# Performance work log

Hardware: AMD Instinct MI355X
Metric: run time of the kernel (lower is better)

Reference implementation:

```python
import jax, jax.numpy as jnp
import numpy as np

NP = 14      # patches per side
PS = 16      # patch size
L = 12       # transformer blocks
H = 12       # heads
DH = 64      # head dim
D = 768      # hidden dim
S = NP * NP + 1  # 197 tokens
EPS = 1e-5   # torch LayerNorm default eps


def _pos_embed():
    # pos[i, j] = sin(i / 10000^(2*(j//2)/D)) for even j, cos(...) for odd j
    i = jnp.arange(S, dtype=jnp.float32)[:, None]
    j = jnp.arange(D)
    angle = i / jnp.power(jnp.float32(10000.0), (2.0 * (j // 2).astype(jnp.float32)) / D)
    return jnp.where(j % 2 == 0, jnp.sin(angle), jnp.cos(angle))  # [S, D]


def _ln(x, g, b):
    m = jnp.mean(x, axis=-1, keepdims=True)
    v = jnp.mean((x - m) ** 2, axis=-1, keepdims=True)
    return (x - m) / jnp.sqrt(v + EPS) * g + b


def setup_inputs() -> dict:
    key = jax.random.key(0)
    ks = iter(jax.random.split(key, 16))
    r = lambda shape, s=0.02: jax.random.normal(next(ks), shape, dtype=jnp.float32) * s
    return {
        'image': jax.random.normal(next(ks), (32, 3, 224, 224), dtype=jnp.float32),
        'W_embed': r((D, 3 * PS * PS)),
        'b_embed': jnp.zeros((D,), jnp.float32),
        'cls': r((1, D), 1.0),
        'Wq': r((L, H, DH, DH)), 'bq': jnp.zeros((L, H, DH), jnp.float32),
        'Wk': r((L, H, DH, DH)), 'bk': jnp.zeros((L, H, DH), jnp.float32),
        'Wv': r((L, H, DH, DH)), 'bv': jnp.zeros((L, H, DH), jnp.float32),
        'ln1_g': jnp.ones((L, D), jnp.float32), 'ln1_b': jnp.zeros((L, D), jnp.float32),
        'ln2_g': jnp.ones((L, D), jnp.float32), 'ln2_b': jnp.zeros((L, D), jnp.float32),
        'W1': r((L, 4 * D, D)), 'b1': jnp.zeros((L, 4 * D), jnp.float32),
        'W2': r((L, D, 4 * D)), 'b2': jnp.zeros((L, D), jnp.float32),
        'Wh': r((1000, D)), 'bh': jnp.zeros((1000,), jnp.float32),
    }


def reference(image, W_embed, b_embed, cls, Wq, bq, Wk, bk, Wv, bv,
              ln1_g, ln1_b, ln2_g, ln2_b, W1, b1, W2, b2, Wh, bh):
    B = image.shape[0]
    # patchify: (B,C,H,W) -> (B, NP*NP, C*PS*PS), token order row-major over (i,j), flatten order (C,ps,ps)
    patches = image.reshape(B, 3, NP, PS, NP, PS).transpose(0, 2, 4, 1, 3, 5).reshape(B, NP * NP, 3 * PS * PS)
    tokens = patches @ W_embed.T + b_embed                      # [B, 196, D]
    tokens = jnp.concatenate([jnp.broadcast_to(cls[None], (B, 1, D)), tokens], axis=1)  # [B, S, D]
    x = tokens + _pos_embed()[None]
    scale = 1.0 / jnp.sqrt(jnp.float32(DH))
    for l in range(L):
        h = _ln(x, ln1_g[l], ln1_b[l]).reshape(B, S, H, DH)
        q = jnp.einsum('bshd,hed->bshe', h, Wq[l]) + bq[l]
        k = jnp.einsum('bshd,hed->bshe', h, Wk[l]) + bk[l]
        v = jnp.einsum('bshd,hed->bshe', h, Wv[l]) + bv[l]
        att = jax.nn.softmax(jnp.einsum('bshe,bthe->bhst', q, k) * scale, axis=-1)
        o = jnp.einsum('bhst,bthe->bshe', att, v).reshape(B, S, D)
        x = x + o
        h2 = _ln(x, ln2_g[l], ln2_b[l])
        m = jax.nn.gelu(h2 @ W1[l].T + b1[l], approximate=False)  # torch nn.GELU = exact erf
        x = x + m @ W2[l].T + b2[l]
    return x[:, 0] @ Wh.T + bh  # [B, 1000]
```

## Files before the change

### kernel.cpp

```cpp
#include <hip/hip_runtime.h>
#include <math.h>

#define BB 32
#define SS 197
#define DD 768
#define HH 12
#define DHD 64
#define LL 12
#define FF 3072
#define NPATCH 196
#define NTOK (BB * SS)
#define MPAD 6400
#define LNEPS 1e-5f

typedef short bf8_t __attribute__((ext_vector_type(8)));
typedef float f4_t  __attribute__((ext_vector_type(4)));
typedef unsigned short u16x8 __attribute__((ext_vector_type(8)));

__device__ __forceinline__ unsigned short f2bf(float x) {
    unsigned u = __float_as_uint(x);
    return (unsigned short)((u + 0x8000u) >> 16);
}
__device__ __forceinline__ float bf_lo(unsigned u) { return __uint_as_float(u << 16); }

__device__ __forceinline__ void gl_lds16(const void* g, void* l) {
    __builtin_amdgcn_global_load_lds((const __attribute__((address_space(1))) unsigned int*)g,
                                     (__attribute__((address_space(3))) unsigned int*)l, 16, 0, 0);
}

__global__ __launch_bounds__(256) void k_conv(const float* __restrict__ a,
                                              unsigned short* __restrict__ o, int n4) {
    for (int i = blockIdx.x * 256 + threadIdx.x; i < n4; i += gridDim.x * 256) {
        float4 v = ((const float4*)a)[i];
        ushort4 r;
        r.x = f2bf(v.x); r.y = f2bf(v.y); r.z = f2bf(v.z); r.w = f2bf(v.w);
        ((ushort4*)o)[i] = r;
    }
}

__global__ __launch_bounds__(256) void k_conv2(const float* __restrict__ a1,
                                               unsigned short* __restrict__ o1, int n1,
                                               const float* __restrict__ a2,
                                               unsigned short* __restrict__ o2, int n2) {
    for (int i = blockIdx.x * 256 + threadIdx.x; i < n1 + n2; i += gridDim.x * 256) {
        const float* a = (i < n1) ? a1 : a2;
        unsigned short* o = (i < n1) ? o1 : o2;
        int j = (i < n1) ? i : i - n1;
        float4 v = ((const float4*)a)[j];
        ushort4 r;
        r.x = f2bf(v.x); r.y = f2bf(v.y); r.z = f2bf(v.z); r.w = f2bf(v.w);
        ((ushort4*)o)[j] = r;
    }
}

__global__ __launch_bounds__(256) void k_patchify(const float* __restrict__ img,
                                                  unsigned short* __restrict__ P) {
    const int total = BB * NPATCH * DD;
    for (int idx = blockIdx.x * 256 + threadIdx.x; idx < total; idx += gridDim.x * 256) {
        int e = idx % DD;
        int rest = idx / DD;
        int p = rest % NPATCH;
        int b = rest / NPATCH;
        int c = e >> 8;
        int pi = (e >> 4) & 15;
        int pj = e & 15;
        int i = p / 14, j = p % 14;
        P[idx] = f2bf(img[(((size_t)b * 3 + c) * 224 + (i * 16 + pi)) * 224 + (j * 16 + pj)]);
    }
}

template <int EPI>
__global__ __launch_bounds__(256) void k_gemm_bf(const unsigned short* __restrict__ A,
                                                 const unsigned short* __restrict__ Bw,
                                                 const float* __restrict__ bias,
                                                 void* __restrict__ Cout,
                                                 int M, int N, int K) {
    __shared__ unsigned short As[128 * 32];
    __shared__ unsigned short Bs[128 * 32];
    const int tid = threadIdx.x;
    const int wave = tid >> 6, lane = tid & 63;
    const int m0 = blockIdx.y << 7, n0 = blockIdx.x << 7;

    const int r0 = tid >> 2, kp = (tid & 3) * 8;
    const unsigned short* gA0 = A + (size_t)(m0 + r0) * K + kp;
    const unsigned short* gA1 = A + (size_t)(m0 + 64 + r0) * K + kp;
    const unsigned short* gB0 = Bw + (size_t)(n0 + r0) * K + kp;
    const unsigned short* gB1 = Bw + (size_t)(n0 + 64 + r0) * K + kp;
    unsigned short* lA0 = &As[tid * 8];
    unsigned short* lA1 = &As[(tid + 256) * 8];
    unsigned short* lB0 = &Bs[tid * 8];
    unsigned short* lB1 = &Bs[(tid + 256) * 8];

    const int mh = (wave >> 1) << 6, nh = (wave & 1) << 6;
    const int lm = lane & 15, kq = lane >> 4;

    f4_t acc[4][4];
#pragma unroll
    for (int i = 0; i < 4; ++i)
#pragma unroll
        for (int j = 0; j < 4; ++j) acc[i][j] = (f4_t){0.f, 0.f, 0.f, 0.f};

    for (int k0 = 0; k0 < K; k0 += 32) {
        gl_lds16(gA0, lA0);
        gl_lds16(gA1, lA1);
        gl_lds16(gB0, lB0);
        gl_lds16(gB1, lB1);
        gA0 += 32; gA1 += 32; gB0 += 32; gB1 += 32;
        __syncthreads();
        bf8_t af[4], bfr[4];
#pragma unroll
        for (int mt = 0; mt < 4; ++mt)
            af[mt] = *(const bf8_t*)&As[(mh + mt * 16 + lm) * 32 + kq * 8];
#pragma unroll
        for (int nt = 0; nt < 4; ++nt)
            bfr[nt] = *(const bf8_t*)&Bs[(nh + nt * 16 + lm) * 32 + kq * 8];
#pragma unroll
        for (int mt = 0; mt < 4; ++mt)
#pragma unroll
            for (int nt = 0; nt < 4; ++nt)
                acc[mt][nt] = __builtin_amdgcn_mfma_f32_16x16x32_bf16(af[mt], bfr[nt],
                                                                      acc[mt][nt], 0, 0, 0);
        __syncthreads();
    }

    const int rbase = m0 + mh + kq * 4;
    const int cbase = n0 + nh + lm;
#pragma unroll
    for (int mt = 0; mt < 4; ++mt) {
#pragma unroll
        for (int nt = 0; nt < 4; ++nt) {
            const int col = cbase + nt * 16;
            const float bv = bias[col];
#pragma unroll
            for (int r = 0; r < 4; ++r) {
                const int row = rbase + mt * 16 + r;
                float val = acc[mt][nt][r] + bv;
                if (EPI == 0) {
                    size_t om = (size_t)(row / 196) * 197 + (row % 196) + 1;
                    ((float*)Cout)[om * DD + col] = val;
                } else if (EPI == 1) {
                    val = 0.5f * val * (1.f + erff(val * 0.7071067811865476f));
                    ((unsigned short*)Cout)[(size_t)row * N + col] = f2bf(val);
                } else {
                    if (row < M) ((float*)Cout)[(size_t)row * DD + col] += val;
                }
            }
        }
    }
}

__global__ __launch_bounds__(256) void k_gemm_sk(const unsigned short* __restrict__ A,
                                                 const unsigned short* __restrict__ Bw,
                                                 const float* __restrict__ bias,
                                                 float* __restrict__ Cout,
                                                 int M, int N, int K) {
    __shared__ unsigned short As[128 * 32];
    __shared__ unsigned short Bs[128 * 32];
    const int tid = threadIdx.x;
    const int wave = tid >> 6, lane = tid & 63;
    const int m0 = blockIdx.y << 7, n0 = blockIdx.x << 7;
    const int ksplit = K / gridDim.z;
    const int kbeg = blockIdx.z * ksplit;

    const int r0 = tid >> 2, kp = (tid & 3) * 8;
    const unsigned short* gA0 = A + (size_t)(m0 + r0) * K + kbeg + kp;
    const unsigned short* gA1 = A + (size_t)(m0 + 64 + r0) * K + kbeg + kp;
    const unsigned short* gB0 = Bw + (size_t)(n0 + r0) * K + kbeg + kp;
    const unsigned short* gB1 = Bw + (size_t)(n0 + 64 + r0) * K + kbeg + kp;
    unsigned short* lA0 = &As[tid * 8];
    unsigned short* lA1 = &As[(tid + 256) * 8];
    unsigned short* lB0 = &Bs[tid * 8];
    unsigned short* lB1 = &Bs[(tid + 256) * 8];

    const int mh = (wave >> 1) << 6, nh = (wave & 1) << 6;
    const int lm = lane & 15, kq = lane >> 4;

    f4_t acc[4][4];
#pragma unroll
    for (int i = 0; i < 4; ++i)
#pragma unroll
        for (int j = 0; j < 4; ++j) acc[i][j] = (f4_t){0.f, 0.f, 0.f, 0.f};

    for (int k0 = 0; k0 < ksplit; k0 += 32) {
        gl_lds16(gA0, lA0);
        gl_lds16(gA1, lA1);
        gl_lds16(gB0, lB0);
        gl_lds16(gB1, lB1);
        gA0 += 32; gA1 += 32; gB0 += 32; gB1 += 32;
        __syncthreads();
        bf8_t af[4], bfr[4];
#pragma unroll
        for (int mt = 0; mt < 4; ++mt)
            af[mt] = *(const bf8_t*)&As[(mh + mt * 16 + lm) * 32 + kq * 8];
#pragma unroll
        for (int nt = 0; nt < 4; ++nt)
            bfr[nt] = *(const bf8_t*)&Bs[(nh + nt * 16 + lm) * 32 + kq * 8];
#pragma unroll
        for (int mt = 0; mt < 4; ++mt)
#pragma unroll
            for (int nt = 0; nt < 4; ++nt)
                acc[mt][nt] = __builtin_amdgcn_mfma_f32_16x16x32_bf16(af[mt], bfr[nt],
                                                                      acc[mt][nt], 0, 0, 0);
        __syncthreads();
    }

    const int rbase = m0 + mh + kq * 4;
    const int cbase = n0 + nh + lm;
    const bool addb = (blockIdx.z == 0);
#pragma unroll
    for (int mt = 0; mt < 4; ++mt) {
#pragma unroll
        for (int nt = 0; nt < 4; ++nt) {
            const int col = cbase + nt * 16;
            const float bv = addb ? bias[col] : 0.f;
#pragma unroll
            for (int r = 0; r < 4; ++r) {
                const int row = rbase + mt * 16 + r;
                if (row < M)
                    unsafeAtomicAdd(&Cout[(size_t)row * DD + col], acc[mt][nt][r] + bv);
            }
        }
    }
}

__global__ __launch_bounds__(256) void k_qkv_mfma(const unsigned short* __restrict__ h,
                                                  const unsigned short* __restrict__ Wqb,
                                                  const unsigned short* __restrict__ Wkb,
                                                  const unsigned short* __restrict__ Wvb,
                                                  const float* __restrict__ bq,
                                                  const float* __restrict__ bk,
                                                  const float* __restrict__ bv,
                                                  unsigned short* __restrict__ qo,
                                                  unsigned short* __restrict__ ko,
                                                  unsigned short* __restrict__ vo) {
    __shared__ unsigned short As[2 * 128 * 32];
    __shared__ unsigned short Bs[3 * 2 * 64 * 32];
    const int head = blockIdx.x;
    const int m0 = blockIdx.y << 7;
    const int tid = threadIdx.x;
    const int wave = tid >> 6, lane = tid & 63;
    const int lm = lane & 15, kq = lane >> 4;

#pragma unroll
    for (int j = 0; j < 4; ++j) {
        int khalf = j >> 1;
        int rem = (j & 1) * 256 + tid;
        int row = rem >> 2, koff = (rem & 3) * 8;
        gl_lds16(h + (size_t)(m0 + row) * DD + head * 64 + khalf * 32 + koff,
                 &As[(j * 256 + tid) * 8]);
    }
    const unsigned short* Wq_h = Wqb + head * 4096;
    const unsigned short* Wk_h = Wkb + head * 4096;
    const unsigned short* Wv_h = Wvb + head * 4096;
#pragma unroll
    for (int j = 0; j < 6; ++j) {
        const unsigned short* src = (j < 2) ? Wq_h : ((j < 4) ? Wk_h : Wv_h);
        int cm = (j & 1) * 256 + tid;
        int khalf = cm >> 8;
        int rem2 = cm & 255;
        int row = rem2 >> 2, koff = (rem2 & 3) * 8;
        gl_lds16(src + row * 64 + khalf * 32 + koff, &Bs[(j * 256 + tid) * 8]);
    }
    __syncthreads();

    f4_t acc[2][12];
#pragma unroll
    for (int i = 0; i < 2; ++i)
#pragma unroll
        for (int j = 0; j < 12; ++j) acc[i][j] = (f4_t){0.f, 0.f, 0.f, 0.f};

#pragma unroll
    for (int kh = 0; kh < 2; ++kh) {
        bf8_t af[2], bfr[12];
#pragma unroll
        for (int mt = 0; mt < 2; ++mt)
            af[mt] = *(const bf8_t*)&As[kh * 4096 + (wave * 32 + mt * 16 + lm) * 32 + kq * 8];
#pragma unroll
        for (int nt = 0; nt < 12; ++nt)
            bfr[nt] = *(const bf8_t*)&Bs[(nt >> 2) * 4096 + kh * 2048 +
                                         ((nt & 3) * 16 + lm) * 32 + kq * 8];
#pragma unroll
        for (int mt = 0; mt < 2; ++mt)
#pragma unroll
            for (int nt = 0; nt < 12; ++nt)
                acc[mt][nt] = __builtin_amdgcn_mfma_f32_16x16x32_bf16(af[mt], bfr[nt],
                                                                      acc[mt][nt], 0, 0, 0);
    }

    const int rbase = m0 + wave * 32 + kq * 4;
#pragma unroll
    for (int mt = 0; mt < 2; ++mt) {
#pragma unroll
        for (int nt = 0; nt < 12; ++nt) {
            const int col = nt * 16 + lm;
            const int e = col & 63;
            const float* bsrc = (nt < 4) ? bq : ((nt < 8) ? bk : bv);
            unsigned short* dst = (nt < 4) ? qo : ((nt < 8) ? ko : vo);
            const float bval = bsrc[head * 64 + e];
#pragma unroll
            for (int r = 0; r < 4; ++r) {
                const int row = rbase + mt * 16 + r;
                if (row < NTOK)
                    dst[(size_t)row * DD + head * 64 + e] = f2bf(acc[mt][nt][r] + bval);
            }
        }
    }
}

__global__ __launch_bounds__(256) void k_posadd(float* __restrict__ x,
                                                const float* __restrict__ cls) {
    const int total = BB * SS * DD;
    const float LN1E4 = 9.210340371976184f;
    for (int idx = blockIdx.x * 256 + threadIdx.x; idx < total; idx += gridDim.x * 256) {
        int d = idx % DD;
        int s = (idx / DD) % SS;
        float ang = (float)s * __expf(-LN1E4 * (float)(2 * (d >> 1)) / 768.f);
        float pv = (d & 1) ? __cosf(ang) : __sinf(ang);
        if (s == 0) x[idx] = cls[d] + pv;
        else        x[idx] += pv;
    }
}

__global__ __launch_bounds__(256) void k_ln2(const float* __restrict__ x,
                                             const float* __restrict__ g,
                                             const float* __restrict__ bp,
                                             unsigned short* __restrict__ out) {
    const int row = blockIdx.x * 4 + (threadIdx.x >> 6);
    const int lane = threadIdx.x & 63;
    if (row >= NTOK) return;
    const float* xr = x + (size_t)row * DD + lane * 12;
    float4 a = ((const float4*)xr)[0];
    float4 b = ((const float4*)xr)[1];
    float4 c = ((const float4*)xr)[2];
    float s = a.x + a.y + a.z + a.w + b.x + b.y + b.z + b.w + c.x + c.y + c.z + c.w;
#pragma unroll
    for (int o = 32; o; o >>= 1) s += __shfl_xor(s, o);
    const float mean = s * (1.f / DD);
    float vr = 0.f, e0;
    e0 = a.x - mean; vr += e0 * e0; e0 = a.y - mean; vr += e0 * e0;
    e0 = a.z - mean; vr += e0 * e0; e0 = a.w - mean; vr += e0 * e0;
    e0 = b.x - mean; vr += e0 * e0; e0 = b.y - mean; vr += e0 * e0;
    e0 = b.z - mean; vr += e0 * e0; e0 = b.w - mean; vr += e0 * e0;
    e0 = c.x - mean; vr += e0 * e0; e0 = c.y - mean; vr += e0 * e0;
    e0 = c.z - mean; vr += e0 * e0; e0 = c.w - mean; vr += e0 * e0;
#pragma unroll
    for (int o = 32; o; o >>= 1) vr += __shfl_xor(vr, o);
    const float rstd = rsqrtf(vr * (1.f / DD) + LNEPS);

    const float4* g4 = (const float4*)(g + lane * 12);
    const float4* b4p = (const float4*)(bp + lane * 12);
    unsigned short* op = out + (size_t)row * DD + lane * 12;
    float4 gv, bv;
    ushort4 r;
    gv = g4[0]; bv = b4p[0];
    r.x = f2bf((a.x - mean) * rstd * gv.x + bv.x);
    r.y = f2bf((a.y - mean) * rstd * gv.y + bv.y);
    r.z = f2bf((a.z - mean) * rstd * gv.z + bv.z);
    r.w = f2bf((a.w - mean) * rstd * gv.w + bv.w);
    ((ushort4*)op)[0] = r;
    gv = g4[1]; bv = b4p[1];
    r.x = f2bf((b.x - mean) * rstd * gv.x + bv.x);
    r.y = f2bf((b.y - mean) * rstd * gv.y + bv.y);
    r.z = f2bf((b.z - mean) * rstd * gv.z + bv.z);
    r.w = f2bf((b.w - mean) * rstd * gv.w + bv.w);
    ((ushort4*)op)[1] = r;
    gv = g4[2]; bv = b4p[2];
    r.x = f2bf((c.x - mean) * rstd * gv.x + bv.x);
    r.y = f2bf((c.y - mean) * rstd * gv.y + bv.y);
    r.z = f2bf((c.z - mean) * rstd * gv.z + bv.z);
    r.w = f2bf((c.w - mean) * rstd * gv.w + bv.w);
    ((ushort4*)op)[2] = r;
}

__global__ __launch_bounds__(256) void k_attn3(const unsigned short* __restrict__ qg,
                                               const unsigned short* __restrict__ kg,
                                               const unsigned short* __restrict__ vg,
                                               float* __restrict__ x) {
    const int qt = blockIdx.x, head = blockIdx.y, b = blockIdx.z;
    const int tid = threadIdx.x, wv = tid >> 6, lane = tid & 63;
    const int lm = lane & 15, kq = lane >> 4;

    __shared__ __align__(16) unsigned short lds[29696];
    unsigned short* Kl = lds;
    unsigned short* Pl = lds;
    unsigned short* Vt = lds + 14848;

    const size_t tokbase = (size_t)b * SS;
    const unsigned short* kb = kg + tokbase * DD + head * 64;
    const unsigned short* vb = vg + tokbase * DD + head * 64;
    const unsigned short* qb = qg + tokbase * DD + head * 64;

#pragma unroll
    for (int it = 0; it < 7; ++it) {
        int c = it * 256 + tid;
        int kh = c / 896, rem = c - kh * 896;
        int t = rem >> 2, cc = rem & 3;
        gl_lds16(kb + (size_t)t * DD + kh * 32 + cc * 8, (char*)lds + c * 16);
    }
#pragma unroll
    for (int it = 0; it < 7; ++it) {
        int idx = it * 256 + tid;
        int t = idx >> 3, eg = idx & 7;
        if (t < SS) {
            u16x8 v8 = *(const u16x8*)(vb + (size_t)t * DD + eg * 8);
#pragma unroll
            for (int j = 0; j < 8; ++j) Vt[(eg * 8 + j) * 232 + t] = v8[j];
        } else {
#pragma unroll
            for (int j = 0; j < 8; ++j) Vt[(eg * 8 + j) * 232 + t] = 0;
        }
    }

    const int qrow = qt * 64 + wv * 16 + lm;
    bf8_t qf0 = *(const bf8_t*)(qb + (size_t)qrow * DD + kq * 8);
    bf8_t qf1 = *(const bf8_t*)(qb + (size_t)qrow * DD + 32 + kq * 8);

    __syncthreads();

    f4_t sacc[13];
#pragma unroll
    for (int tt = 0; tt < 13; ++tt) sacc[tt] = (f4_t){0.f, 0.f, 0.f, 0.f};
#pragma unroll
    for (int tt = 0; tt < 13; ++tt) {
        bf8_t a0 = *(const bf8_t*)&Kl[(tt * 16 + lm) * 32 + kq * 8];
        bf8_t a1 = *(const bf8_t*)&Kl[7168 + (tt * 16 + lm) * 32 + kq * 8];
        sacc[tt] = __builtin_amdgcn_mfma_f32_16x16x32_bf16(a0, qf0, sacc[tt], 0, 0, 0);
        sacc[tt] = __builtin_amdgcn_mfma_f32_16x16x32_bf16(a1, qf1, sacc[tt], 0, 0, 0);
    }

    float mx = -1e30f;
#pragma unroll
    for (int tt = 0; tt < 13; ++tt)
#pragma unroll
        for (int r = 0; r < 4; ++r) {
            float s = sacc[tt][r] * 0.125f;
            if (tt == 12 && (kq * 4 + r) >= 5) s = -1e30f;
            sacc[tt][r] = s;
            mx = fmaxf(mx, s);
        }
    mx = fmaxf(mx, __shfl_xor(mx, 16));
    mx = fmaxf(mx, __shfl_xor(mx, 32));
    float sum = 0.f;
#pragma unroll
    for (int tt = 0; tt < 13; ++tt)
#pragma unroll
        for (int r = 0; r < 4; ++r) {
            float p = __expf(sacc[tt][r] - mx);
            sacc[tt][r] = p;
            sum += p;
        }
    sum += __shfl_xor(sum, 16);
    sum += __shfl_xor(sum, 32);
    const float inv = 1.f / sum;

    __syncthreads();

    unsigned short* Pw = Pl + wv * 3712;
#pragma unroll
    for (int tt = 0; tt < 13; ++tt)
#pragma unroll
        for (int r = 0; r < 4; ++r)
            Pw[lm * 232 + tt * 16 + kq * 4 + r] = f2bf(sacc[tt][r]);
    *(short4*)&Pw[lm * 232 + 208 + kq * 4] = make_short4(0, 0, 0, 0);

    f4_t oacc[4];
#pragma unroll
    for (int et = 0; et < 4; ++et) oacc[et] = (f4_t){0.f, 0.f, 0.f, 0.f};
#pragma unroll
    for (int kc = 0; kc < 7; ++kc) {
        bf8_t pa = *(const bf8_t*)&Pw[lm * 232 + kc * 32 + kq * 8];
#pragma unroll
        for (int et = 0; et < 4; ++et) {
            bf8_t vv = *(const bf8_t*)&Vt[(et * 16 + lm) * 232 + kc * 32 + kq * 8];
            oacc[et] = __builtin_amdgcn_mfma_f32_16x16x32_bf16(pa, vv, oacc[et], 0, 0, 0);
        }
    }

    float invq[4];
#pragma unroll
    for (int r = 0; r < 4; ++r) invq[r] = __shfl(inv, kq * 4 + r);

    float* xp = x + tokbase * DD + head * 64;
#pragma unroll
    for (int r = 0; r < 4; ++r) {
        const int qgr = qt * 64 + wv * 16 + kq * 4 + r;
        if (qgr < SS) {
#pragma unroll
            for (int et = 0; et < 4; ++et)
                xp[(size_t)qgr * DD + et * 16 + lm] += oacc[et][r] * invq[r];
        }
    }
}

__global__ __launch_bounds__(256) void k_head(const float* __restrict__ x,
                                              const float* __restrict__ Wh,
                                              const float* __restrict__ bh,
                                              float* __restrict__ out) {
    const int b = blockIdx.y;
    const int c = blockIdx.x * 256 + threadIdx.x;
    __shared__ __align__(16) float xs[DD];
    const float* xr = x + (size_t)b * SS * DD;
    for (int d = threadIdx.x; d < DD; d += 256) xs[d] = xr[d];
    __syncthreads();
    if (c < 1000) {
        const float4* w4 = (const float4*)(Wh + (size_t)c * DD);
        float acc = 0.f;
#pragma unroll 4
        for (int d4 = 0; d4 < DD / 4; ++d4) {
            float4 w = w4[d4];
            const float4 xv = *(const float4*)&xs[d4 << 2];
            acc += xv.x * w.x + xv.y * w.y + xv.z * w.z + xv.w * w.w;
        }
        out[(size_t)b * 1000 + c] = acc + bh[c];
    }
}

extern "C" void kernel_launch(void* const* d_in, const int* in_sizes, int n_in,
                              void* d_out, int out_size, void* d_ws, size_t ws_size,
                              hipStream_t stream) {
    const float* image   = (const float*)d_in[0];
    const float* W_embed = (const float*)d_in[1];
    const float* b_embed = (const float*)d_in[2];
    const float* cls     = (const float*)d_in[3];
    const float* Wq      = (const float*)d_in[4];
    const float* bq      = (const float*)d_in[5];
    const float* Wk      = (const float*)d_in[6];
    const float* bk      = (const float*)d_in[7];
    const float* Wv      = (const float*)d_in[8];
    const float* bv      = (const float*)d_in[9];
    const float* ln1g    = (const float*)d_in[10];
    const float* ln1b    = (const float*)d_in[11];
    const float* ln2g    = (const float*)d_in[12];
    const float* ln2b    = (const float*)d_in[13];
    const float* W1      = (const float*)d_in[14];
    const float* b1      = (const float*)d_in[15];
    const float* W2      = (const float*)d_in[16];
    const float* b2      = (const float*)d_in[17];
    const float* Wh      = (const float*)d_in[18];
    const float* bh      = (const float*)d_in[19];
    float* out = (float*)d_out;

    float* x = (float*)d_ws;
    unsigned short* h_bf   = (unsigned short*)(x + (size_t)NTOK * DD);
    unsigned short* q_bf   = h_bf + (size_t)MPAD * DD;
    unsigned short* k_bf   = q_bf + (size_t)MPAD * DD;
    unsigned short* v_bf   = k_bf + (size_t)MPAD * DD;
    unsigned short* mlp_bf = v_bf + (size_t)MPAD * DD;
    unsigned short* W1_bf  = mlp_bf + (size_t)MPAD * FF;
    unsigned short* W2_bf  = W1_bf + (size_t)FF * DD;
    unsigned short* We_bf  = W2_bf + (size_t)FF * DD;
    unsigned short* Wq_bf  = We_bf + (size_t)DD * DD;
    unsigned short* Wk_bf  = Wq_bf + (size_t)LL * HH * DHD * DHD;
    unsigned short* Wv_bf  = Wk_bf + (size_t)LL * HH * DHD * DHD;
    unsigned short* P_bf   = mlp_bf;

    const int QKVW = LL * HH * DHD * DHD;

    k_conv<<<576, 256, 0, stream>>>(W_embed, We_bf, DD * DD / 4);
    k_conv<<<576, 256, 0, stream>>>(Wq, Wq_bf, QKVW / 4);
    k_conv<<<576, 256, 0, stream>>>(Wk, Wk_bf, QKVW / 4);
    k_conv<<<576, 256, 0, stream>>>(Wv, Wv_bf, QKVW / 4);

    k_patchify<<<1024, 256, 0, stream>>>(image, P_bf);
    k_gemm_bf<0><<<dim3(6, 49), 256, 0, stream>>>(P_bf, We_bf, b_embed, x,
                                                  BB * NPATCH, DD, DD);
    k_posadd<<<1024, 256, 0, stream>>>(x, cls);

    for (int l = 0; l < LL; ++l) {
        k_ln2<<<(NTOK + 3) / 4, 256, 0, stream>>>(x, ln1g + l * DD, ln1b + l * DD, h_bf);
        k_qkv_mfma<<<dim3(HH, MPAD / 128), 256, 0, stream>>>(
            h_bf, Wq_bf + (size_t)l * HH * 4096, Wk_bf + (size_t)l * HH * 4096,
            Wv_bf + (size_t)l * HH * 4096, bq + l * DD, bk + l * DD, bv + l * DD,
            q_bf, k_bf, v_bf);
        k_attn3<<<dim3(4, HH, BB), 256, 0, stream>>>(q_bf, k_bf, v_bf, x);
        k_ln2<<<(NTOK + 3) / 4, 256, 0, stream>>>(x, ln2g + l * DD, ln2b + l * DD, h_bf);
        k_conv2<<<2048, 256, 0, stream>>>(W1 + (size_t)l * FF * DD, W1_bf, FF * DD / 4,
                                          W2 + (size_t)l * DD * FF, W2_bf, FF * DD / 4);
        k_gemm_bf<1><<<dim3(FF / 128, MPAD / 128), 256, 0, stream>>>(
            h_bf, W1_bf, b1 + (size_t)l * FF, mlp_bf, NTOK, FF, DD);
        k_gemm_sk<<<dim3(DD / 128, MPAD / 128, 2), 256, 0, stream>>>(
            mlp_bf, W2_bf, b2 + (size_t)l * DD, x, NTOK, DD, FF);
    }

    k_head<<<dim3(4, BB), 256, 0, stream>>>(x, Wh, bh, out);
}
```

Measured before the change: 2.937 ms.

## Double-buffer GEMM LDS tiles, swizzle LDS layout, XCD-remap blocks, split-K 4

Both GEMM kernels now use two LDS buffers so the global-to-LDS load of the next K tile overlaps the MFMA work on the current one, with manual vmcnt/lgkmcnt waits and raw barriers. The K-chunk placement in LDS is XOR-swizzled by row to cut bank conflicts on fragment reads. Block IDs are remapped so neighbouring tiles land on the same XCD for L2 reuse. The W2 GEMM split-K goes from 2 to 4, adding more atomic adds into x in exchange for more parallelism. LDS use per block doubles, which may lower occupancy.

After: 3.112 ms. 5.9% more time.

```diff
diff --git a/kernel.cpp b/kernel.cpp
--- a/kernel.cpp
+++ b/kernel.cpp
@@ -1,5 +1,6 @@
 #include <hip/hip_runtime.h>
 #include <math.h>
+
 
 #define BB 32
 #define SS 197
@@ -26,6 +27,12 @@
 __device__ __forceinline__ void gl_lds16(const void* g, void* l) {
     __builtin_amdgcn_global_load_lds((const __attribute__((address_space(1))) unsigned int*)g,
                                      (__attribute__((address_space(3))) unsigned int*)l, 16, 0, 0);
+}
+
+__device__ __forceinline__ int xcd_swz(int bid, int nwg) {
+    const int q = nwg >> 3, r = nwg & 7;
+    const int xcd = bid & 7, idx = bid >> 3;
+    return (xcd < r ? xcd * (q + 1) : r * (q + 1) + (xcd - r) * q) + idx;
 }
 
 __global__ __launch_bounds__(256) void k_conv(const float* __restrict__ a,
@@ -75,24 +82,26 @@
                                                  const float* __restrict__ bias,
                                                  void* __restrict__ Cout,
                                                  int M, int N, int K) {
-    __shared__ unsigned short As[128 * 32];
-    __shared__ unsigned short Bs[128 * 32];
+    __shared__ unsigned short As[2][128 * 32];
+    __shared__ unsigned short Bs[2][128 * 32];
     const int tid = threadIdx.x;
     const int wave = tid >> 6, lane = tid & 63;
-    const int m0 = blockIdx.y << 7, n0 = blockIdx.x << 7;
-
-    const int r0 = tid >> 2, kp = (tid & 3) * 8;
+
+    const int nwg = gridDim.x * gridDim.y;
+    const int sb = xcd_swz(blockIdx.y * gridDim.x + blockIdx.x, nwg);
+    const int bx = sb % gridDim.x, by = sb / gridDim.x;
+    const int m0 = by << 7, n0 = bx << 7;
+
+    const int r0 = tid >> 2;
+    const int kp = (((tid & 3) ^ ((r0 >> 1) & 3)) << 3);
     const unsigned short* gA0 = A + (size_t)(m0 + r0) * K + kp;
     const unsigned short* gA1 = A + (size_t)(m0 + 64 + r0) * K + kp;
     const unsigned short* gB0 = Bw + (size_t)(n0 + r0) * K + kp;
     const unsigned short* gB1 = Bw + (size_t)(n0 + 64 + r0) * K + kp;
-    unsigned short* lA0 = &As[tid * 8];
-    unsigned short* lA1 = &As[(tid + 256) * 8];
-    unsigned short* lB0 = &Bs[tid * 8];
-    unsigned short* lB1 = &Bs[(tid + 256) * 8];
 
     const int mh = (wave >> 1) << 6, nh = (wave & 1) << 6;
     const int lm = lane & 15, kq = lane >> 4;
+    const int kqx = ((kq ^ ((lm >> 1) & 3)) << 3);
 
     f4_t acc[4][4];
 #pragma unroll
@@ -100,27 +109,44 @@
 #pragma unroll
         for (int j = 0; j < 4; ++j) acc[i][j] = (f4_t){0.f, 0.f, 0.f, 0.f};
 
-    for (int k0 = 0; k0 < K; k0 += 32) {
-        gl_lds16(gA0, lA0);
-        gl_lds16(gA1, lA1);
-        gl_lds16(gB0, lB0);
-        gl_lds16(gB1, lB1);
-        gA0 += 32; gA1 += 32; gB0 += 32; gB1 += 32;
-        __syncthreads();
+    const int nt = K >> 5;
+    gl_lds16(gA0, &As[0][tid * 8]);
+    gl_lds16(gA1, &As[0][(tid + 256) * 8]);
+    gl_lds16(gB0, &Bs[0][tid * 8]);
+    gl_lds16(gB1, &Bs[0][(tid + 256) * 8]);
+    gA0 += 32; gA1 += 32; gB0 += 32; gB1 += 32;
+
+    for (int t = 0; t < nt; ++t) {
+        const int cur = t & 1;
+        if (t + 1 < nt) {
+            const int nxb = cur ^ 1;
+            gl_lds16(gA0, &As[nxb][tid * 8]);
+            gl_lds16(gA1, &As[nxb][(tid + 256) * 8]);
+            gl_lds16(gB0, &Bs[nxb][tid * 8]);
+            gl_lds16(gB1, &Bs[nxb][(tid + 256) * 8]);
+            gA0 += 32; gA1 += 32; gB0 += 32; gB1 += 32;
+            asm volatile("s_waitcnt vmcnt(4)" ::: "memory");
+        } else {
+            asm volatile("s_waitcnt vmcnt(0)" ::: "memory");
+        }
+        __builtin_amdgcn_s_barrier();
+        __builtin_amdgcn_sched_barrier(0);
         bf8_t af[4], bfr[4];
 #pragma unroll
         for (int mt = 0; mt < 4; ++mt)
-            af[mt] = *(const bf8_t*)&As[(mh + mt * 16 + lm) * 32 + kq * 8];
-#pragma unroll
-        for (int nt = 0; nt < 4; ++nt)
-            bfr[nt] = *(const bf8_t*)&Bs[(nh + nt * 16 + lm) * 32 + kq * 8];
+            af[mt] = *(const bf8_t*)&As[cur][(mh + mt * 16 + lm) * 32 + kqx];
+#pragma unroll
+        for (int nv = 0; nv < 4; ++nv)
+            bfr[nv] = *(const bf8_t*)&Bs[cur][(nh + nv * 16 + lm) * 32 + kqx];
 #pragma unroll
         for (int mt = 0; mt < 4; ++mt)
 #pragma unroll
-            for (int nt = 0; nt < 4; ++nt)
-                acc[mt][nt] = __builtin_amdgcn_mfma_f32_16x16x32_bf16(af[mt], bfr[nt],
-                                                                      acc[mt][nt], 0, 0, 0);
-        __syncthreads();
+            for (int nv = 0; nv < 4; ++nv)
+                acc[mt][nv] = __builtin_amdgcn_mfma_f32_16x16x32_bf16(af[mt], bfr[nv],
+                                                                      acc[mt][nv], 0, 0, 0);
+        asm volatile("s_waitcnt lgkmcnt(0)" ::: "memory");
+        __builtin_amdgcn_sched_barrier(0);
+        __builtin_amdgcn_s_barrier();
     }
 
     const int rbase = m0 + mh + kq * 4;
@@ -128,13 +154,13 @@
 #pragma unroll
     for (int mt = 0; mt < 4; ++mt) {
 #pragma unroll
-        for (int nt = 0; nt < 4; ++nt) {
-            const int col = cbase + nt * 16;
+        for (int nv = 0; nv < 4; ++nv) {
+            const int col = cbase + nv * 16;
             const float bv = bias[col];
 #pragma unroll
             for (int r = 0; r < 4; ++r) {
                 const int row = rbase + mt * 16 + r;
-                float val = acc[mt][nt][r] + bv;
+                float val = acc[mt][nv][r] + bv;
                 if (EPI == 0) {
                     size_t om = (size_t)(row / 196) * 197 + (row % 196) + 1;
                     ((float*)Cout)[om * DD + col] = val;
@@ -154,26 +180,32 @@
                                                  const float* __restrict__ bias,
                                                  float* __restrict__ Cout,
                                                  int M, int N, int K) {
-    __shared__ unsigned short As[128 * 32];
-    __shared__ unsigned short Bs[128 * 32];
+    __shared__ unsigned short As[2][128 * 32];
+    __shared__ unsigned short Bs[2][128 * 32];
     const int tid = threadIdx.x;
     const int wave = tid >> 6, lane = tid & 63;
-    const int m0 = blockIdx.y << 7, n0 = blockIdx.x << 7;
+
+    const int nwg = gridDim.x * gridDim.y * gridDim.z;
+    const int bid = (blockIdx.z * gridDim.y + blockIdx.y) * gridDim.x + blockIdx.x;
+    const int sb = xcd_swz(bid, nwg);
+    const int bx = sb % gridDim.x;
+    const int rest = sb / gridDim.x;
+    const int by = rest % gridDim.y;
+    const int bz = rest / gridDim.y;
+    const int m0 = by << 7, n0 = bx << 7;
     const int ksplit = K / gridDim.z;
-    const int kbeg = blockIdx.z * ksplit;
-
-    const int r0 = tid >> 2, kp = (tid & 3) * 8;
+    const int kbeg = bz * ksplit;
+
+    const int r0 = tid >> 2;
+    const int kp = (((tid & 3) ^ ((r0 >> 1) & 3)) << 3);
     const unsigned short* gA0 = A + (size_t)(m0 + r0) * K + kbeg + kp;
     const unsigned short* gA1 = A + (size_t)(m0 + 64 + r0) * K + kbeg + kp;
     const unsigned short* gB0 = Bw + (size_t)(n0 + r0) * K + kbeg + kp;
     const unsigned short* gB1 = Bw + (size_t)(n0 + 64 + r0) * K + kbeg + kp;
-    unsigned short* lA0 = &As[tid * 8];
-    unsigned short* lA1 = &As[(tid + 256) * 8];
-    unsigned short* lB0 = &Bs[tid * 8];
-    unsigned short* lB1 = &Bs[(tid + 256) * 8];
 
     const int mh = (wave >> 1) << 6, nh = (wave & 1) << 6;
     const int lm = lane & 15, kq = lane >> 4;
+    const int kqx = ((kq ^ ((lm >> 1) & 3)) << 3);
 
     f4_t acc[4][4];
 #pragma unroll
@@ -181,43 +213,60 @@
 #pragma unroll
         for (int j = 0; j < 4; ++j) acc[i][j] = (f4_t){0.f, 0.f, 0.f, 0.f};
 
-    for (int k0 = 0; k0 < ksplit; k0 += 32) {
-        gl_lds16(gA0, lA0);
-        gl_lds16(gA1, lA1);
-        gl_lds16(gB0, lB0);
-        gl_lds16(gB1, lB1);
-        gA0 += 32; gA1 += 32; gB0 += 32; gB1 += 32;
-        __syncthreads();
+    const int nt = ksplit >> 5;
+    gl_lds16(gA0, &As[0][tid * 8]);
+    gl_lds16(gA1, &As[0][(tid + 256) * 8]);
+    gl_lds16(gB0, &Bs[0][tid * 8]);
+    gl_lds16(gB1, &Bs[0][(tid + 256) * 8]);
+    gA0 += 32; gA1 += 32; gB0 += 32; gB1 += 32;
+
+    for (int t = 0; t < nt; ++t) {
+        const int cur = t & 1;
+        if (t + 1 < nt) {
+            const int nxb = cur ^ 1;
+            gl_lds16(gA0, &As[nxb][tid * 8]);
+            gl_lds16(gA1, &As[nxb][(tid + 256) * 8]);
+            gl_lds16(gB0, &Bs[nxb][tid * 8]);
+            gl_lds16(gB1, &Bs[nxb][(tid + 256) * 8]);
+            gA0 += 32; gA1 += 32; gB0 += 32; gB1 += 32;
+            asm volatile("s_waitcnt vmcnt(4)" ::: "memory");
+        } else {
+            asm volatile("s_waitcnt vmcnt(0)" ::: "memory");
+        }
+        __builtin_amdgcn_s_barrier();
+        __builtin_amdgcn_sched_barrier(0);
         bf8_t af[4], bfr[4];
 #pragma unroll
         for (int mt = 0; mt < 4; ++mt)
-            af[mt] = *(const bf8_t*)&As[(mh + mt * 16 + lm) * 32 + kq * 8];
-#pragma unroll
-        for (int nt = 0; nt < 4; ++nt)
-            bfr[nt] = *(const bf8_t*)&Bs[(nh + nt * 16 + lm) * 32 + kq * 8];
+            af[mt] = *(const bf8_t*)&As[cur][(mh + mt * 16 + lm) * 32 + kqx];
+#pragma unroll
+        for (int nv = 0; nv < 4; ++nv)
+            bfr[nv] = *(const bf8_t*)&Bs[cur][(nh + nv * 16 + lm) * 32 + kqx];
 #pragma unroll
         for (int mt = 0; mt < 4; ++mt)
 #pragma unroll
-            for (int nt = 0; nt < 4; ++nt)
-                acc[mt][nt] = __builtin_amdgcn_mfma_f32_16x16x32_bf16(af[mt], bfr[nt],
-                                                                      acc[mt][nt], 0, 0, 0);
-        __syncthreads();
+            for (int nv = 0; nv < 4; ++nv)
+                acc[mt][nv] = __builtin_amdgcn_mfma_f32_16x16x32_bf16(af[mt], bfr[nv],
+                                                                      acc[mt][nv], 0, 0, 0);
+        asm volatile("s_waitcnt lgkmcnt(0)" ::: "memory");
+        __builtin_amdgcn_sched_barrier(0);
+        __builtin_amdgcn_s_barrier();
     }
 
     const int rbase = m0 + mh + kq * 4;
     const int cbase = n0 + nh + lm;
-    const bool addb = (blockIdx.z == 0);
+    const bool addb = (bz == 0);
 #pragma unroll
     for (int mt = 0; mt < 4; ++mt) {
 #pragma unroll
-        for (int nt = 0; nt < 4; ++nt) {
-            const int col = cbase + nt * 16;
+        for (int nv = 0; nv < 4; ++nv) {
+            const int col = cbase + nv * 16;
             const float bv = addb ? bias[col] : 0.f;
 #pragma unroll
             for (int r = 0; r < 4; ++r) {
                 const int row = rbase + mt * 16 + r;
                 if (row < M)
-                    unsafeAtomicAdd(&Cout[(size_t)row * DD + col], acc[mt][nt][r] + bv);
+                    unsafeAtomicAdd(&Cout[(size_t)row * DD + col], acc[mt][nv][r] + bv);
             }
         }
     }
@@ -578,7 +627,7 @@
                                           W2 + (size_t)l * DD * FF, W2_bf, FF * DD / 4);
         k_gemm_bf<1><<<dim3(FF / 128, MPAD / 128), 256, 0, stream>>>(
             h_bf, W1_bf, b1 + (size_t)l * FF, mlp_bf, NTOK, FF, DD);
-        k_gemm_sk<<<dim3(DD / 128, MPAD / 128, 2), 256, 0, stream>>>(
+        k_gemm_sk<<<dim3(DD / 128, MPAD / 128, 4), 256, 0, stream>>>(
             mlp_bf, W2_bf, b2 + (size_t)l * DD, x, NTOK, DD, FF);
     }
 
```
